# Kernel tuning notes

Measured on AMD Instinct MI355X. Metric: run time of the kernel, lower is better.

## Reference

```python
import jax, jax.numpy as jnp
import numpy as np

N = 100000
E = 1250000
D = 64
R = 16


def _glorot(key, shape):
    fan_in, fan_out = shape[-2], shape[-1]
    lim = jnp.sqrt(6.0 / (fan_in + fan_out))
    return jax.random.uniform(key, shape, jnp.float32, -lim, lim)


def setup_inputs() -> dict:
    key = jax.random.key(0)
    ks = jax.random.split(key, 9)
    x = jax.random.normal(ks[0], (N, D), jnp.float32)
    edge_index = jax.random.randint(ks[1], (2, E), 0, N, jnp.int64 if jax.config.jax_enable_x64 else jnp.int32).astype(jnp.int32)
    edge_type = jax.random.randint(ks[2], (E,), 0, R).astype(jnp.int32)
    return {
        "x": x,
        "edge_index": edge_index,
        "edge_type": edge_type,
        "W1": _glorot(ks[3], (R, D, D)),
        "sw1": _glorot(ks[4], (D, D)),
        "b1": jnp.zeros((D,), jnp.float32),
        "W2": _glorot(ks[5], (R, D, D)),
        "sw2": _glorot(ks[6], (D, D)),
        "b2": jnp.zeros((D,), jnp.float32),
    }


def _rgcn_layer(x, src, dst, edge_type, W, sw, b, residual):
    # self transform [N, O]
    out = x @ sw
    # per-relation transform of all nodes: [N, R, O] (avoids [E, D, O] gathered weights,
    # same math as bmm(x_j, W[edge_type]))
    xW = jnp.einsum('nd,rdo->nro', x, W)
    msg = xW[src, edge_type]                      # [E, O] per-edge messages
    agg = jax.ops.segment_sum(msg, dst, num_segments=N)  # scatter-add aggregate
    out = out + agg
    if residual:
        out = out + x  # Identity residual (in == out channels)
    out = out + b
    return jax.nn.relu(out)


def reference(x, edge_index, edge_type, W1, sw1, b1, W2, sw2, b2):
    src, dst = edge_index[0], edge_index[1]
    # layer 1: residual=True; layer 2: encoding=False -> no residual.
    # activation (relu) applied after every layer by RGCN.forward; dropout p=0 / eval -> no-op.
    h = _rgcn_layer(x, src, dst, edge_type, W1, sw1, b1, residual=True)
    h = _rgcn_layer(h, src, dst, edge_type, W2, sw2, b2, residual=False)
    return h
```

## Files before the change

kernel.cpp:

```cpp
#include <hip/hip_runtime.h>
#include <hip/hip_bf16.h>

#define NN 100000
#define NE 1250000
#define DD 64
#define RR 16
#define NTILE 6250
#define NBINS 100000
#define NBLK_SCAN 391

typedef __attribute__((ext_vector_type(8))) short s16x8;
typedef __attribute__((ext_vector_type(4))) float f32x4;

static __device__ __forceinline__ unsigned short f2bf(float v) {
    __hip_bfloat16 h = __float2bfloat16(v);
    return __builtin_bit_cast(unsigned short, h);
}
static __device__ __forceinline__ unsigned int pack2(float a, float b) {
    return ((unsigned int)f2bf(b) << 16) | (unsigned int)f2bf(a);
}


__global__ void hist_key(const int* __restrict__ dst, const int* __restrict__ et,
                         int* __restrict__ cnt) {
    int e = blockIdx.x * 256 + threadIdx.x;
    if (e < NE) atomicAdd(&cnt[(dst[e] >> 4) * 16 + et[e]], 1);
}

__global__ __launch_bounds__(256) void scan1(const int* __restrict__ cnt,
                                             int* __restrict__ rp, int* __restrict__ part) {
    __shared__ int s[256];
    int i = blockIdx.x * 256 + threadIdx.x;
    int v = (i < NBINS) ? cnt[i] : 0;
    s[threadIdx.x] = v;
    __syncthreads();
    for (int off = 1; off < 256; off <<= 1) {
        int t = (threadIdx.x >= off) ? s[threadIdx.x - off] : 0;
        __syncthreads();
        s[threadIdx.x] += t;
        __syncthreads();
    }
    if (i < NBINS) rp[i] = s[threadIdx.x] - v;
    if (threadIdx.x == 255) part[blockIdx.x] = s[255];
}

__global__ void scan2(int* __restrict__ part, int* __restrict__ rp) {
    __shared__ int s[NBLK_SCAN];
    if (threadIdx.x < NBLK_SCAN) s[threadIdx.x] = part[threadIdx.x];
    __syncthreads();
    if (threadIdx.x == 0) {
        int acc = 0;
        for (int b = 0; b < NBLK_SCAN; ++b) { int t = s[b]; s[b] = acc; acc += t; }
        rp[NBINS] = NE;
    }
    __syncthreads();
    if (threadIdx.x < NBLK_SCAN) part[threadIdx.x] = s[threadIdx.x];
}

__global__ void scan3(int* __restrict__ rp, const int* __restrict__ part, int* __restrict__ cur) {
    int i = blockIdx.x * 256 + threadIdx.x;
    if (i < NBINS) {
        int v = rp[i] + part[blockIdx.x];
        rp[i] = v;
        cur[i] = v;
    }
}

__global__ void scatter_key(const int* __restrict__ src, const int* __restrict__ dst,
                            const int* __restrict__ et, int* __restrict__ cur,
                            unsigned int* __restrict__ ep) {
    int e = blockIdx.x * 256 + threadIdx.x;
    if (e >= NE) return;
    int d = dst[e];
    int p = atomicAdd(&cur[(d >> 4) * 16 + et[e]], 1);
    ep[p] = (unsigned int)src[e] | ((unsigned int)(d & 15) << 20);
}


__global__ void prep_w2(const float* __restrict__ W1, const float* __restrict__ sw1,
                        const float* __restrict__ W2, const float* __restrict__ sw2,
                        unsigned short* __restrict__ wt) {
    int i = blockIdx.x * 256 + threadIdx.x;
    if (i >= 2 * 17 * DD * DD) return;
    int d = i & 63;
    int o = (i >> 6) & 63;
    int p = (i >> 12) % 17;
    int l = i / (17 * DD * DD);
    const float* srcp;
    if (p < 16) srcp = (l ? W2 : W1) + p * DD * DD;
    else        srcp = (l ? sw2 : sw1);
    wt[i] = f2bf(srcp[d * DD + o]);
}

__global__ void prep_x2(const float* __restrict__ x, unsigned short* __restrict__ xb) {
    int i = blockIdx.x * blockDim.x + threadIdx.x;
    if (i < NN * DD) xb[i] = f2bf(x[i]);
}

__global__ __launch_bounds__(256) void fused_layer(
    const unsigned short* __restrict__ xb,
    const unsigned short* __restrict__ wt,
    const int* __restrict__ rp,
    const unsigned int* __restrict__ ep,
    const float* __restrict__ bias,
    const float* __restrict__ xres,
    unsigned short* __restrict__ outb,
    float* __restrict__ outf)
{
    __shared__ float stage[4][16 * DD];
    const int wid  = threadIdx.x >> 6;
    const int lane = threadIdx.x & 63;
    const int c = lane & 15;
    const int q = lane >> 4;
    const int tile = blockIdx.x * 4 + wid;
    if (tile >= NTILE) return;
    const int n0 = tile * 16;

    const int sA = ((c >> 2) << 3) + (c & 3);

    f32x4 D[4];
    #pragma unroll
    for (int ob = 0; ob < 4; ++ob) D[ob] = (f32x4){0.f, 0.f, 0.f, 0.f};

    for (int r = 0; r < 17; ++r) {
        int s0, s1;
        if (r < 16) { s0 = rp[tile * 16 + r]; s1 = rp[tile * 16 + r + 1]; }
        else        { s0 = 0; s1 = 16; }
        const unsigned short* wp = wt + r * (DD * DD);

        for (int b0 = s0; b0 < s1; b0 += 32) {
            int eA = b0 + sA;
            int eB = eA + 4;
            int srcA, srcB, dlA, dlB;
            if (r < 16) {
                unsigned int wa = ep[min(eA, s1 - 1)];
                unsigned int wb = ep[min(eB, s1 - 1)];
                srcA = (int)(wa & 0xFFFFF);
                srcB = (int)(wb & 0xFFFFF);
                dlA = (eA < s1) ? (int)(wa >> 20) : 31;
                dlB = (eB < s1) ? (int)(wb >> 20) : 31;
            } else {
                dlA = (eA < 16) ? eA : 31;
                dlB = (eB < 16) ? eB : 31;
                srcA = n0 + ((eA < 16) ? eA : 0);
                srcB = n0 + ((eB < 16) ? eB : 0);
            }

            const unsigned short* xrA = xb + (size_t)srcA * DD + q * 8;
            const unsigned short* xrB = xb + (size_t)srcB * DD + q * 8;
            s16x8 aA0 = *(const s16x8*)(xrA);
            s16x8 aA1 = *(const s16x8*)(xrA + 32);
            s16x8 aB0 = *(const s16x8*)(xrB);
            s16x8 aB1 = *(const s16x8*)(xrB + 32);

            s16x8 a2;
            #pragma unroll
            for (int j = 0; j < 4; ++j) {
                int dj = __shfl(dlA, q * 4 + j, 64);
                a2[j] = (dj == c) ? (short)0x3F80 : (short)0;
            }
            #pragma unroll
            for (int j = 0; j < 4; ++j) {
                int dj = __shfl(dlB, q * 4 + j, 64);
                a2[j + 4] = (dj == c) ? (short)0x3F80 : (short)0;
            }

            #pragma unroll
            for (int ob = 0; ob < 4; ++ob) {
                const unsigned short* wrow = wp + (ob * 16 + c) * DD + q * 8;
                s16x8 w0 = *(const s16x8*)(wrow);
                s16x8 w1 = *(const s16x8*)(wrow + 32);
                f32x4 cA = {0.f, 0.f, 0.f, 0.f};
                cA = __builtin_amdgcn_mfma_f32_16x16x32_bf16(aA0, w0, cA, 0, 0, 0);
                cA = __builtin_amdgcn_mfma_f32_16x16x32_bf16(aA1, w1, cA, 0, 0, 0);
                f32x4 cB = {0.f, 0.f, 0.f, 0.f};
                cB = __builtin_amdgcn_mfma_f32_16x16x32_bf16(aB0, w0, cB, 0, 0, 0);
                cB = __builtin_amdgcn_mfma_f32_16x16x32_bf16(aB1, w1, cB, 0, 0, 0);
                s16x8 b2;
                #pragma unroll
                for (int j = 0; j < 4; ++j) {
                    b2[j]     = (short)f2bf(cA[j]);
                    b2[j + 4] = (short)f2bf(cB[j]);
                }
                D[ob] = __builtin_amdgcn_mfma_f32_16x16x32_bf16(a2, b2, D[ob], 0, 0, 0);
            }
        }
    }

    float* ls = stage[wid];
    #pragma unroll
    for (int ob = 0; ob < 4; ++ob) {
        const int ch = ob * 16 + c;
        #pragma unroll
        for (int v = 0; v < 4; ++v) {
            const int node = q * 4 + v;
            float val = D[ob][v] + bias[ch];
            if (xres) val += xres[(size_t)(n0 + node) * DD + ch];
            val = fmaxf(val, 0.f);
            ls[node * DD + ch] = val;
        }
    }
    if (outb) {
        unsigned short* g = outb + (size_t)n0 * DD;
        #pragma unroll
        for (int j = 0; j < 4; ++j) {
            int i4 = lane + 64 * j;
            const float* p = ls + i4 * 4;
            uint2 pk;
            pk.x = pack2(p[0], p[1]);
            pk.y = pack2(p[2], p[3]);
            *(uint2*)(g + (size_t)i4 * 4) = pk;
        }
    }
    if (outf) {
        float* g = outf + (size_t)n0 * DD;
        #pragma unroll
        for (int j = 0; j < 4; ++j) {
            int i4 = lane + 64 * j;
            const float4* p = (const float4*)(ls + i4 * 4);
            *(float4*)(g + (size_t)i4 * 4) = *p;
        }
    }
}


extern "C" void kernel_launch(void* const* d_in, const int* in_sizes, int n_in,
                              void* d_out, int out_size, void* d_ws, size_t ws_size,
                              hipStream_t stream)
{
    (void)in_sizes; (void)n_in; (void)out_size; (void)ws_size;
    const float* x    = (const float*)d_in[0];
    const int*   ei   = (const int*)d_in[1];
    const int*   et   = (const int*)d_in[2];
    const float* W1   = (const float*)d_in[3];
    const float* sw1  = (const float*)d_in[4];
    const float* b1   = (const float*)d_in[5];
    const float* W2   = (const float*)d_in[6];
    const float* sw2  = (const float*)d_in[7];
    const float* b2   = (const float*)d_in[8];
    float* out = (float*)d_out;

    const int* srcA = ei;
    const int* dstA = ei + NE;

    char* ws = (char*)d_ws;
    unsigned short* xb   = (unsigned short*)(ws);
    unsigned short* h1b  = (unsigned short*)(ws + 12800000);
    unsigned short* wt2  = (unsigned short*)(ws + 25600000);
    unsigned int*   ep   = (unsigned int*)(ws + 25878528);
    int*            rp   = (int*)(ws + 30878528);
    int*            cnt  = (int*)(ws + 31278544);
    int*            cur  = (int*)(ws + 31678544);
    int*            part = (int*)(ws + 32078544);

    const int NB_E    = (NE + 255) / 256;
    const int NB_ELEM = (NN * DD + 255) / 256;
    const int WPL = 17 * DD * DD;

    hipMemsetAsync(cnt, 0, NBINS * sizeof(int), stream);
    hist_key<<<NB_E, 256, 0, stream>>>(dstA, et, cnt);
    scan1<<<NBLK_SCAN, 256, 0, stream>>>(cnt, rp, part);
    scan2<<<1, 512, 0, stream>>>(part, rp);
    scan3<<<NBLK_SCAN, 256, 0, stream>>>(rp, part, cur);
    scatter_key<<<NB_E, 256, 0, stream>>>(srcA, dstA, et, cur, ep);

    prep_w2<<<(2 * 17 * DD * DD + 255) / 256, 256, 0, stream>>>(W1, sw1, W2, sw2, wt2);
    prep_x2<<<NB_ELEM, 256, 0, stream>>>(x, xb);

    const int NB_F = (NTILE + 3) / 4;

    fused_layer<<<NB_F, 256, 0, stream>>>(xb, wt2, rp, ep, b1, x, h1b, nullptr);
    fused_layer<<<NB_F, 256, 0, stream>>>(h1b, wt2 + WPL, rp, ep, b2, nullptr, nullptr, out);
}
```

Before: 546.7 us.

## Split relations of each node tile across four waves with LDS reduction

```diff
diff --git a/kernel.cpp b/kernel.cpp
--- a/kernel.cpp
+++ b/kernel.cpp
@@ -8,6 +8,7 @@
 #define NTILE 6250
 #define NBINS 100000
 #define NBLK_SCAN 391
+#define EBCAP 512
 
 typedef __attribute__((ext_vector_type(8))) short s16x8;
 typedef __attribute__((ext_vector_type(4))) float f32x4;
@@ -107,51 +108,62 @@
     unsigned short* __restrict__ outb,
     float* __restrict__ outf)
 {
-    __shared__ float stage[4][16 * DD];
-    const int wid  = threadIdx.x >> 6;
-    const int lane = threadIdx.x & 63;
+    __shared__ unsigned int eb[EBCAP];
+    __shared__ int rps[17];
+    __shared__ float Dred[4 * 1024];
+    const int tid  = threadIdx.x;
+    const int wid  = tid >> 6;
+    const int lane = tid & 63;
     const int c = lane & 15;
     const int q = lane >> 4;
-    const int tile = blockIdx.x * 4 + wid;
-    if (tile >= NTILE) return;
+    const int tile = blockIdx.x;
     const int n0 = tile * 16;
 
-    const int sA = ((c >> 2) << 3) + (c & 3);
+    if (tid < 17) rps[tid] = rp[tile * 16 + tid];
+    __syncthreads();
+    const int e0 = rps[0];
+    const int cntT = rps[16] - e0;
+    const bool inLds = (cntT <= EBCAP);
+    const int nst = min(cntT, EBCAP);
+    for (int i = tid; i < nst; i += 256) eb[i] = ep[e0 + i];
+    __syncthreads();
 
     f32x4 D[4];
     #pragma unroll
     for (int ob = 0; ob < 4; ++ob) D[ob] = (f32x4){0.f, 0.f, 0.f, 0.f};
 
-    for (int r = 0; r < 17; ++r) {
+    for (int r = wid; r < 17; r += 4) {
+        const unsigned short* wp = wt + r * (DD * DD);
         int s0, s1;
-        if (r < 16) { s0 = rp[tile * 16 + r]; s1 = rp[tile * 16 + r + 1]; }
-        else        { s0 = 0; s1 = 16; }
-        const unsigned short* wp = wt + r * (DD * DD);
+        if (r < 16) { s0 = rps[r]; s1 = rps[r + 1]; } else { s0 = 0; s1 = 16; }
 
         for (int b0 = s0; b0 < s1; b0 += 32) {
-            int eA = b0 + sA;
-            int eB = eA + 4;
-            int srcA, srcB, dlA, dlB;
+            const int rem = s1 - b0;
+            int srcA, dlA;
             if (r < 16) {
-                unsigned int wa = ep[min(eA, s1 - 1)];
-                unsigned int wb = ep[min(eB, s1 - 1)];
+                int eA = min(b0 + c, s1 - 1);
+                unsigned int wa = inLds ? eb[eA - e0] : ep[eA];
                 srcA = (int)(wa & 0xFFFFF);
+                dlA  = (b0 + c < s1) ? (int)(wa >> 20) : 31;
+            } else { srcA = n0 + c; dlA = c; }
+            const bool hasB = (rem > 16);
+            int srcB = srcA, dlB = 31;
+            if (hasB) {
+                int eB = min(b0 + 16 + c, s1 - 1);
+                unsigned int wb = inLds ? eb[eB - e0] : ep[eB];
                 srcB = (int)(wb & 0xFFFFF);
-                dlA = (eA < s1) ? (int)(wa >> 20) : 31;
-                dlB = (eB < s1) ? (int)(wb >> 20) : 31;
-            } else {
-                dlA = (eA < 16) ? eA : 31;
-                dlB = (eB < 16) ? eB : 31;
-                srcA = n0 + ((eA < 16) ? eA : 0);
-                srcB = n0 + ((eB < 16) ? eB : 0);
+                dlB  = (b0 + 16 + c < s1) ? (int)(wb >> 20) : 31;
             }
 
             const unsigned short* xrA = xb + (size_t)srcA * DD + q * 8;
-            const unsigned short* xrB = xb + (size_t)srcB * DD + q * 8;
             s16x8 aA0 = *(const s16x8*)(xrA);
             s16x8 aA1 = *(const s16x8*)(xrA + 32);
-            s16x8 aB0 = *(const s16x8*)(xrB);
-            s16x8 aB1 = *(const s16x8*)(xrB + 32);
+            s16x8 aB0, aB1;
+            if (hasB) {
+                const unsigned short* xrB = xb + (size_t)srcB * DD + q * 8;
+                aB0 = *(const s16x8*)(xrB);
+                aB1 = *(const s16x8*)(xrB + 32);
+            }
 
             s16x8 a2;
             #pragma unroll
@@ -159,10 +171,15 @@
                 int dj = __shfl(dlA, q * 4 + j, 64);
                 a2[j] = (dj == c) ? (short)0x3F80 : (short)0;
             }
-            #pragma unroll
-            for (int j = 0; j < 4; ++j) {
-                int dj = __shfl(dlB, q * 4 + j, 64);
-                a2[j + 4] = (dj == c) ? (short)0x3F80 : (short)0;
+            if (hasB) {
+                #pragma unroll
+                for (int j = 0; j < 4; ++j) {
+                    int dj = __shfl(dlB, q * 4 + j, 64);
+                    a2[j + 4] = (dj == c) ? (short)0x3F80 : (short)0;
+                }
+            } else {
+                #pragma unroll
+                for (int j = 0; j < 4; ++j) a2[j + 4] = 0;
             }
 
             #pragma unroll
@@ -173,52 +190,57 @@
                 f32x4 cA = {0.f, 0.f, 0.f, 0.f};
                 cA = __builtin_amdgcn_mfma_f32_16x16x32_bf16(aA0, w0, cA, 0, 0, 0);
                 cA = __builtin_amdgcn_mfma_f32_16x16x32_bf16(aA1, w1, cA, 0, 0, 0);
-                f32x4 cB = {0.f, 0.f, 0.f, 0.f};
-                cB = __builtin_amdgcn_mfma_f32_16x16x32_bf16(aB0, w0, cB, 0, 0, 0);
-                cB = __builtin_amdgcn_mfma_f32_16x16x32_bf16(aB1, w1, cB, 0, 0, 0);
                 s16x8 b2;
-                #pragma unroll
-                for (int j = 0; j < 4; ++j) {
-                    b2[j]     = (short)f2bf(cA[j]);
-                    b2[j + 4] = (short)f2bf(cB[j]);
+                if (hasB) {
+                    f32x4 cB = {0.f, 0.f, 0.f, 0.f};
+                    cB = __builtin_amdgcn_mfma_f32_16x16x32_bf16(aB0, w0, cB, 0, 0, 0);
+                    cB = __builtin_amdgcn_mfma_f32_16x16x32_bf16(aB1, w1, cB, 0, 0, 0);
+                    #pragma unroll
+                    for (int j = 0; j < 4; ++j) {
+                        b2[j]     = (short)f2bf(cA[j]);
+                        b2[j + 4] = (short)f2bf(cB[j]);
+                    }
+                } else {
+                    #pragma unroll
+                    for (int j = 0; j < 4; ++j) {
+                        b2[j]     = (short)f2bf(cA[j]);
+                        b2[j + 4] = 0;
+                    }
                 }
                 D[ob] = __builtin_amdgcn_mfma_f32_16x16x32_bf16(a2, b2, D[ob], 0, 0, 0);
             }
         }
     }
 
-    float* ls = stage[wid];
+    {
+        float* dred = Dred + wid * 1024;
+        #pragma unroll
+        for (int ob = 0; ob < 4; ++ob)
+            #pragma unroll
+            for (int v = 0; v < 4; ++v)
+                dred[(q * 4 + v) * 64 + ob * 16 + c] = D[ob][v];
+    }
+    __syncthreads();
+
     #pragma unroll
-    for (int ob = 0; ob < 4; ++ob) {
-        const int ch = ob * 16 + c;
-        #pragma unroll
-        for (int v = 0; v < 4; ++v) {
-            const int node = q * 4 + v;
-            float val = D[ob][v] + bias[ch];
-            if (xres) val += xres[(size_t)(n0 + node) * DD + ch];
-            val = fmaxf(val, 0.f);
-            ls[node * DD + ch] = val;
+    for (int k = 0; k < 2; ++k) {
+        int j = k * 512 + tid * 2;
+        int node = j >> 6, ch = j & 63;
+        float v0 = Dred[j]        + Dred[1024 + j]     + Dred[2048 + j]     + Dred[3072 + j];
+        float v1 = Dred[j + 1]    + Dred[1024 + j + 1] + Dred[2048 + j + 1] + Dred[3072 + j + 1];
+        v0 += bias[ch];
+        v1 += bias[ch + 1];
+        if (xres) {
+            const float2 rv = *(const float2*)(xres + (size_t)(n0 + node) * DD + ch);
+            v0 += rv.x; v1 += rv.y;
         }
-    }
-    if (outb) {
-        unsigned short* g = outb + (size_t)n0 * DD;
-        #pragma unroll
-        for (int j = 0; j < 4; ++j) {
-            int i4 = lane + 64 * j;
-            const float* p = ls + i4 * 4;
-            uint2 pk;
-            pk.x = pack2(p[0], p[1]);
-            pk.y = pack2(p[2], p[3]);
-            *(uint2*)(g + (size_t)i4 * 4) = pk;
-        }
-    }
-    if (outf) {
-        float* g = outf + (size_t)n0 * DD;
-        #pragma unroll
-        for (int j = 0; j < 4; ++j) {
-            int i4 = lane + 64 * j;
-            const float4* p = (const float4*)(ls + i4 * 4);
-            *(float4*)(g + (size_t)i4 * 4) = *p;
+        v0 = fmaxf(v0, 0.f);
+        v1 = fmaxf(v1, 0.f);
+        if (outb)
+            *(unsigned int*)(outb + (size_t)(n0 + node) * DD + ch) = pack2(v0, v1);
+        if (outf) {
+            float2 o = {v0, v1};
+            *(float2*)(outf + (size_t)(n0 + node) * DD + ch) = o;
         }
     }
 }
@@ -267,8 +289,6 @@
     prep_w2<<<(2 * 17 * DD * DD + 255) / 256, 256, 0, stream>>>(W1, sw1, W2, sw2, wt2);
     prep_x2<<<NB_ELEM, 256, 0, stream>>>(x, xb);
 
-    const int NB_F = (NTILE + 3) / 4;
-
-    fused_layer<<<NB_F, 256, 0, stream>>>(xb, wt2, rp, ep, b1, x, h1b, nullptr);
-    fused_layer<<<NB_F, 256, 0, stream>>>(h1b, wt2 + WPL, rp, ep, b2, nullptr, nullptr, out);
-}
+    fused_layer<<<NTILE, 256, 0, stream>>>(xb, wt2, rp, ep, b1, x, h1b, nullptr);
+    fused_layer<<<NTILE, 256, 0, stream>>>(h1b, wt2 + WPL, rp, ep, b2, nullptr, nullptr, out);
+}
```

Result: faster. 491.4 us (-10.1%).
